# Kernel tuning notes

Measured on AMD Instinct MI355X. Metric: run time of the kernel, lower is better.

## Reference

```python
import jax, jax.numpy as jnp
import numpy as np

B, C, IN = 8, 1024, 256
OUT, H, NS, SD = 256, 4, 5, 64
DK = OUT // H


def setup_inputs() -> dict:
    key = jax.random.key(0)
    ks = jax.random.split(key, 16)
    s = lambda k, *shape: jax.random.normal(k, shape, dtype=jnp.float32) * 0.05
    return {
        "x": jax.random.normal(ks[0], (B, C, IN), dtype=jnp.float32),
        "A_prior": jax.random.uniform(ks[1], (C, C), dtype=jnp.float32),
        # lin_project
        "Wp": s(ks[2], IN, OUT), "bp": jnp.zeros((OUT,), jnp.float32),
        # stage_mlp: Linear(IN,128) -> ReLU -> Linear(128,NS)
        "Ws1": s(ks[3], IN, 128), "bs1": jnp.zeros((128,), jnp.float32),
        "Ws2": s(ks[4], 128, NS), "bs2": jnp.zeros((NS,), jnp.float32),
        # mlp_c: Linear(NS,SD) -> ReLU -> Linear(SD,SD)
        "Wc1": s(ks[5], NS, SD), "bc1": jnp.zeros((SD,), jnp.float32),
        "Wc2": s(ks[6], SD, SD), "bc2": jnp.zeros((SD,), jnp.float32),
        # att_scorer: Linear(2*DK+SD, 1, bias=False) -> weight vector
        "att_w": s(ks[7], 2 * DK + SD),
        "lam": jnp.ones((H,), jnp.float32),
    }


def reference(x, A_prior, Wp, bp, Ws1, bs1, Ws2, bs2, Wc1, bc1, Wc2, bc2, att_w, lam):
    # projection -> (B, C, H, DK)
    x_proj = (x @ Wp + bp).reshape(B, C, H, DK)
    # stage logits from mean-pooled features
    s_logits = jax.nn.relu(x.mean(axis=1) @ Ws1 + bs1) @ Ws2 + bs2  # (B, NS)
    s_prob = jax.nn.softmax(s_logits, axis=-1)
    c = jax.nn.relu(s_prob @ Wc1 + bc1) @ Wc2 + bc2  # (B, SD)
    # att_scorer is linear over cat([x_src, x_dst, c]); decompose weight to
    # avoid materializing the (B,C,C,H,2*DK+SD) concat tensor.
    w_src, w_dst, w_c = att_w[:DK], att_w[DK:2 * DK], att_w[2 * DK:]
    src_s = jnp.einsum('bjhd,d->bjh', x_proj, w_src)  # x_src[b,i,j] = x_proj[b,j]
    dst_s = jnp.einsum('bihd,d->bih', x_proj, w_dst)  # x_dst[b,i,j] = x_proj[b,i]
    c_s = c @ w_c                                      # (B,)
    e = jax.nn.leaky_relu(
        src_s[:, None, :, :] + dst_s[:, :, None, :] + c_s[:, None, None, None],
        negative_slope=0.2)                            # (B, C, C, H)
    prior = lam[None, None, None, :] * jnp.log(A_prior[None, :, :, None] + 1e-9)
    alpha = jax.nn.softmax(e + prior, axis=2)          # softmax over src j
    out = jnp.einsum('bijh,bjhd->bihd', alpha, x_proj).reshape(B, C, OUT)
    return out, s_logits
```

## Files before the change

kernel.cpp:

```cpp
#include <hip/hip_runtime.h>
#include <hip/hip_fp16.h>

typedef _Float16 f16x8 __attribute__((ext_vector_type(8)));
typedef _Float16 f16x4 __attribute__((ext_vector_type(4)));
typedef float f32x4 __attribute__((ext_vector_type(4)));

#define NB 8
#define NNS 5


__global__ __launch_bounds__(256) void k_prew(const float* __restrict__ Wp,
                                              __half* __restrict__ WpTh) {
  const int k = blockIdx.x;
  const int f = threadIdx.x;
  WpTh[(f << 8) + k] = __float2half(Wp[(k << 8) + f]);
}

__global__ __launch_bounds__(256) void k_mean(const float* __restrict__ x,
                                              float* __restrict__ xmean) {
  const int t = threadIdx.x;
  const int row0 = blockIdx.x << 5;
  const int b = row0 >> 10;
  float ps = 0.f;
  #pragma unroll 8
  for (int r = 0; r < 32; ++r) ps += x[(size_t)(row0 + r) * 256 + t];
  atomicAdd(&xmean[(b << 8) + t], ps);
}

__global__ __launch_bounds__(256, 4) void k_projM(
    const float* __restrict__ x, const __half* __restrict__ WpTh,
    const float* __restrict__ bp, const float* __restrict__ att_w,
    __half* __restrict__ xpT, float* __restrict__ srcP,
    float* __restrict__ dstT) {
  const int t = threadIdx.x;
  const int l = t & 63, w = t >> 6;
  const int lm = l & 15, q = l >> 4;
  const int bm = blockIdx.x >> 2, nh = blockIdx.x & 3;
  const int R0 = (bm << 6) + (w << 4);
  const int f0 = nh << 6;

  const float* arow = x + (size_t)(R0 + lm) * 256 + (q << 3);
  f16x8 ah[8];
  #pragma unroll
  for (int kk = 0; kk < 8; ++kk) {
    const f32x4 xa = *(const f32x4*)(arow + (kk << 5));
    const f32x4 xb = *(const f32x4*)(arow + (kk << 5) + 4);
    f16x8 v;
    #pragma unroll
    for (int u = 0; u < 4; ++u) {
      v[u] = (_Float16)xa[u];
      v[u + 4] = (_Float16)xb[u];
    }
    ah[kk] = v;
  }

  f32x4 acc[4];
  #pragma unroll
  for (int n = 0; n < 4; ++n) acc[n] = (f32x4){0.f, 0.f, 0.f, 0.f};
  #pragma unroll
  for (int n = 0; n < 4; ++n) {
    const __half* brow = WpTh + (size_t)(f0 + (n << 4) + lm) * 256 + (q << 3);
    #pragma unroll
    for (int kk = 0; kk < 8; ++kk) {
      const f16x8 bf = *(const f16x8*)(brow + (kk << 5));
      acc[n] = __builtin_amdgcn_mfma_f32_16x16x32_f16(ah[kk], bf, acc[n],
                                                      0, 0, 0);
    }
  }

  const int b = R0 >> 10;
  const int il = (R0 & 1023) + (q << 2);
  float wsn[4], wdn[4];
  #pragma unroll
  for (int n = 0; n < 4; ++n) {
    const int d = (n << 4) + lm;
    wsn[n] = att_w[d];
    wdn[n] = att_w[64 + d];
  }
  #pragma unroll
  for (int n = 0; n < 4; ++n) {
    const int f = f0 + (n << 4) + lm;
    const float bias = bp[f];
    f16x4 o;
    #pragma unroll
    for (int reg = 0; reg < 4; ++reg) {
      acc[n][reg] += bias;
      o[reg] = (_Float16)acc[n][reg];
    }
    *(f16x4*)(xpT + (((size_t)((b << 8) + f)) << 10) + il) = o;
  }
  #pragma unroll
  for (int reg = 0; reg < 4; ++reg) {
    float ss = 0.f, ds = 0.f;
    #pragma unroll
    for (int n = 0; n < 4; ++n) {
      ss = fmaf(acc[n][reg], wsn[n], ss);
      ds = fmaf(acc[n][reg], wdn[n], ds);
    }
    #pragma unroll
    for (int off = 1; off < 16; off <<= 1) {
      ss += __shfl_xor(ss, off);
      ds += __shfl_xor(ds, off);
    }
    if (lm == 0) {
      const int i = il + reg;
      srcP[((((b << 10) + i)) << 2) + nh] = ss;
      dstT[(((b << 2) + nh) << 10) + i] = ds;
    }
  }
}

__global__ __launch_bounds__(256) void k_head(
    const float* __restrict__ Ws1, const float* __restrict__ bs1,
    const float* __restrict__ Ws2, const float* __restrict__ bs2,
    const float* __restrict__ Wc1, const float* __restrict__ bc1,
    const float* __restrict__ Wc2, const float* __restrict__ bc2,
    const float* __restrict__ att_w, const float* __restrict__ xmean,
    float* __restrict__ cs_ws, float* __restrict__ out_slogits) {
  __shared__ float xm[256];
  __shared__ float h1[128];
  __shared__ float sl[NNS];
  __shared__ float sp[NNS];
  __shared__ float cc1[64];
  __shared__ float cvec[64];
  const int b = blockIdx.x, t = threadIdx.x;
  xm[t] = xmean[b * 256 + t] * (1.f / 1024.f);
  __syncthreads();
  if (t < 128) {
    float a = bs1[t];
    for (int f = 0; f < 256; ++f) a = fmaf(xm[f], Ws1[f * 128 + t], a);
    h1[t] = fmaxf(a, 0.f);
  }
  __syncthreads();
  if (t < NNS) {
    float a = bs2[t];
    for (int k = 0; k < 128; ++k) a = fmaf(h1[k], Ws2[k * NNS + t], a);
    sl[t] = a;
    out_slogits[b * NNS + t] = a;
  }
  __syncthreads();
  if (t == 0) {
    float m = sl[0];
    for (int n = 1; n < NNS; ++n) m = fmaxf(m, sl[n]);
    float s = 0.f;
    for (int n = 0; n < NNS; ++n) { sp[n] = expf(sl[n] - m); s += sp[n]; }
    for (int n = 0; n < NNS; ++n) sp[n] /= s;
  }
  __syncthreads();
  if (t < 64) {
    float a = bc1[t];
    for (int n = 0; n < NNS; ++n) a = fmaf(sp[n], Wc1[n * 64 + t], a);
    cc1[t] = fmaxf(a, 0.f);
  }
  __syncthreads();
  if (t < 64) {
    float a = bc2[t];
    for (int m = 0; m < 64; ++m) a = fmaf(cc1[m], Wc2[m * 64 + t], a);
    cvec[t] = a;
  }
  __syncthreads();
  if (t < 64) {
    float v = cvec[t] * att_w[128 + t];
    #pragma unroll
    for (int m = 32; m; m >>= 1) v += __shfl_xor(v, m);
    if (t == 0) cs_ws[b] = v;
  }
}

__global__ __launch_bounds__(512, 4) void k_attn(
    const __half* __restrict__ xpT, const float* __restrict__ A,
    const float* __restrict__ srcP, const float* __restrict__ dstT,
    const float* __restrict__ cs_ws, const float* __restrict__ lam,
    float* __restrict__ out) {
  __shared__ __align__(16) __half wl[4][16][256];
  __shared__ float dinv[4][16];
  const int t = threadIdx.x;
  const int l = t & 63;
  const int w = t >> 6;
  const int b = blockIdx.x >> 6;
  const int i0 = (blockIdx.x & 63) << 4;
  const float csv = cs_ws[b];
  float lam2[4], dstc[2][4];
  #pragma unroll
  for (int h = 0; h < 4; ++h) {
    lam2[h] = lam[h] * 0.69314718056f;
    #pragma unroll
    for (int rr = 0; rr < 2; ++rr)
      dstc[rr][h] = dstT[(((b << 2) + h) << 10) + i0 + 2 * w + rr] + csv;
  }
  const int r0g = i0 + 2 * w;
  const float* Ar0 = A + (size_t)r0g * 1024;
  const float* Ar1 = Ar0 + 1024;
  char* wlb = (char*)wl;

  const int h2 = w & 3, rh = w >> 2;
  const int lm = l & 15, q = l >> 4;
  f32x4 acc0 = {0.f, 0.f, 0.f, 0.f};
  f32x4 acc1 = {0.f, 0.f, 0.f, 0.f};
  const __half* xb0 =
      xpT + (((size_t)((b << 8) + (h2 << 6) + (rh << 5) + lm)) << 10);
  const __half* xb1 = xb0 + (16 << 10);

  float sums[2][4];
  #pragma unroll
  for (int rr = 0; rr < 2; ++rr)
    #pragma unroll
    for (int h = 0; h < 4; ++h) sums[rr][h] = 0.f;

  for (int cc = 0; cc < 4; ++cc) {
    #pragma unroll
    for (int st = 0; st < 2; ++st) {
      const int jl = (st << 7) + (l << 1);
      const int jg = (cc << 8) + jl;
      const float2 a0 = *(const float2*)(Ar0 + jg);
      const float2 a1 = *(const float2*)(Ar1 + jg);
      const f32x4 sv0 = *(const f32x4*)(srcP + (((b << 10) + jg) << 2));
      const f32x4 sv1 = *(const f32x4*)(srcP + (((b << 10) + jg + 1) << 2));
      float la[2][2];
      la[0][0] = __log2f(a0.x + 1e-9f);
      la[0][1] = __log2f(a0.y + 1e-9f);
      la[1][0] = __log2f(a1.x + 1e-9f);
      la[1][1] = __log2f(a1.y + 1e-9f);
      #pragma unroll
      for (int h = 0; h < 4; ++h) {
        #pragma unroll
        for (int rr = 0; rr < 2; ++rr) {
          __half2 pk;
          #pragma unroll
          for (int jj = 0; jj < 2; ++jj) {
            const float e = (jj ? sv1[h] : sv0[h]) + dstc[rr][h];
            const float lk = fmaxf(e, 0.2f * e);
            const float s = fmaf(lam2[h], la[rr][jj], lk);
            const float p = __expf(s);
            sums[rr][h] += p;
            if (jj) pk.y = __float2half(p); else pk.x = __float2half(p);
          }
          const int row = 2 * w + rr;
          *(__half2*)(wlb + (h << 13) + (row << 9) +
                      ((jl << 1) ^ ((row & 7) << 4))) = pk;
        }
      }
    }
    if (cc == 3) {
      #pragma unroll
      for (int rr = 0; rr < 2; ++rr)
        #pragma unroll
        for (int h = 0; h < 4; ++h) {
          float s = sums[rr][h];
          #pragma unroll
          for (int mm = 32; mm; mm >>= 1) s += __shfl_xor(s, mm);
          sums[rr][h] = s;
        }
      if (l == 0) {
        #pragma unroll
        for (int rr = 0; rr < 2; ++rr)
          #pragma unroll
          for (int h = 0; h < 4; ++h)
            dinv[h][2 * w + rr] = 1.f / sums[rr][h];
      }
    }
    __syncthreads();
    const char* ab = wlb + (h2 << 13) + (lm << 9);
    const int xa = (lm & 7) << 4;
    const __half* xb0c = xb0 + (cc << 8);
    const __half* xb1c = xb1 + (cc << 8);
    #pragma unroll
    for (int kk = 0; kk < 8; ++kk) {
      const int jl2 = (kk << 5) + (q << 3);
      const f16x8 af = *(const f16x8*)(ab + ((jl2 << 1) ^ xa));
      const f16x8 bf0 = *(const f16x8*)(xb0c + jl2);
      const f16x8 bf1 = *(const f16x8*)(xb1c + jl2);
      acc0 = __builtin_amdgcn_mfma_f32_16x16x32_f16(af, bf0, acc0, 0, 0, 0);
      acc1 = __builtin_amdgcn_mfma_f32_16x16x32_f16(af, bf1, acc1, 0, 0, 0);
    }
    __syncthreads();
  }
  float* ob =
      out + (((size_t)((b << 10) + i0)) << 8) + (h2 << 6) + (rh << 5) + lm;
  #pragma unroll
  for (int reg = 0; reg < 4; ++reg) {
    const int mrow = (q << 2) + reg;
    const float dv = dinv[h2][mrow];
    ob[(size_t)mrow << 8] = acc0[reg] * dv;
    ob[((size_t)mrow << 8) + 16] = acc1[reg] * dv;
  }
}

extern "C" void kernel_launch(void* const* d_in, const int* in_sizes, int n_in,
                              void* d_out, int out_size, void* d_ws,
                              size_t ws_size, hipStream_t stream) {
  const float* x     = (const float*)d_in[0];
  const float* A     = (const float*)d_in[1];
  const float* Wp    = (const float*)d_in[2];
  const float* bp    = (const float*)d_in[3];
  const float* Ws1   = (const float*)d_in[4];
  const float* bs1   = (const float*)d_in[5];
  const float* Ws2   = (const float*)d_in[6];
  const float* bs2   = (const float*)d_in[7];
  const float* Wc1   = (const float*)d_in[8];
  const float* bc1   = (const float*)d_in[9];
  const float* Wc2   = (const float*)d_in[10];
  const float* bc2   = (const float*)d_in[11];
  const float* att_w = (const float*)d_in[12];
  const float* lam   = (const float*)d_in[13];
  float* out = (float*)d_out;
  float* ws  = (float*)d_ws;

  __half* xpT  = (__half*)ws;
  float* srcP  = ws + 1048576;
  float* dstT  = ws + 1081344;
  float* xmean = ws + 1114112;
  float* cs    = ws + 1116160;
  __half* WpTh = (__half*)(ws + 1116168);

  hipMemsetAsync(xmean, 0, 2048 * sizeof(float), stream);

  k_prew<<<dim3(256), dim3(256), 0, stream>>>(Wp, WpTh);
  k_mean<<<dim3(256), dim3(256), 0, stream>>>(x, xmean);
  k_projM<<<dim3(512), dim3(256), 0, stream>>>(x, WpTh, bp, att_w, xpT, srcP,
                                               dstT);
  k_head<<<dim3(NB), dim3(256), 0, stream>>>(Ws1, bs1, Ws2, bs2, Wc1, bc1,
                                             Wc2, bc2, att_w, xmean, cs,
                                             out + NB * 1024 * 256);
  k_attn<<<dim3(512), dim3(512), 0, stream>>>(xpT, A, srcP, dstT, cs, lam,
                                              out);
}
```

Measured before the change: 159.5 us.

## Build attention weights in MFMA registers, dropping LDS staging and block syncs

The attention kernel now has each wave compute its softmax probabilities directly in the MFMA A-operand fragment for one head. Source scores move to a head-major layout so they can be loaded as contiguous vectors. This removes the shared-memory weight tile, the __syncthreads barriers and the LDS reduction of row sums; row normalisers are computed with shuffles instead. In exchange, the grid doubles and splits head dims across blocks, so the log/exp of the prior is recomputed per head and per half, which multiplies transcendental work and A-matrix reads. Separately, the weight-transpose and mean kernels are merged into one launch, and the head MLP's first layer is split across all 256 threads.

Measured after the change: 183.9 us. 15.3% more time.

```diff
diff --git a/kernel.cpp b/kernel.cpp
--- a/kernel.cpp
+++ b/kernel.cpp
@@ -9,28 +9,29 @@
 #define NNS 5
 
 
-__global__ __launch_bounds__(256) void k_prew(const float* __restrict__ Wp,
-                                              __half* __restrict__ WpTh) {
-  const int k = blockIdx.x;
-  const int f = threadIdx.x;
-  WpTh[(f << 8) + k] = __float2half(Wp[(k << 8) + f]);
-}
-
-__global__ __launch_bounds__(256) void k_mean(const float* __restrict__ x,
-                                              float* __restrict__ xmean) {
+__global__ __launch_bounds__(256) void k_pre(const float* __restrict__ Wp,
+                                             const float* __restrict__ x,
+                                             __half* __restrict__ WpTh,
+                                             float* __restrict__ xmean) {
   const int t = threadIdx.x;
-  const int row0 = blockIdx.x << 5;
-  const int b = row0 >> 10;
-  float ps = 0.f;
-  #pragma unroll 8
-  for (int r = 0; r < 32; ++r) ps += x[(size_t)(row0 + r) * 256 + t];
-  atomicAdd(&xmean[(b << 8) + t], ps);
+  int blk = blockIdx.x;
+  if (blk < 256) {
+    WpTh[(t << 8) + blk] = __float2half(Wp[(blk << 8) + t]);
+  } else {
+    blk -= 256;
+    const int row0 = blk << 5;
+    const int b = row0 >> 10;
+    float ps = 0.f;
+    #pragma unroll 8
+    for (int r = 0; r < 32; ++r) ps += x[(size_t)(row0 + r) * 256 + t];
+    atomicAdd(&xmean[(b << 8) + t], ps);
+  }
 }
 
 __global__ __launch_bounds__(256, 4) void k_projM(
     const float* __restrict__ x, const __half* __restrict__ WpTh,
     const float* __restrict__ bp, const float* __restrict__ att_w,
-    __half* __restrict__ xpT, float* __restrict__ srcP,
+    __half* __restrict__ xpT, float* __restrict__ srcT,
     float* __restrict__ dstT) {
   const int t = threadIdx.x;
   const int l = t & 63, w = t >> 6;
@@ -104,7 +105,7 @@
     }
     if (lm == 0) {
       const int i = il + reg;
-      srcP[((((b << 10) + i)) << 2) + nh] = ss;
+      srcT[(((b << 2) + nh) << 10) + i] = ss;
       dstT[(((b << 2) + nh) << 10) + i] = ds;
     }
   }
@@ -118,6 +119,7 @@
     const float* __restrict__ att_w, const float* __restrict__ xmean,
     float* __restrict__ cs_ws, float* __restrict__ out_slogits) {
   __shared__ float xm[256];
+  __shared__ float h1p[2][128];
   __shared__ float h1[128];
   __shared__ float sl[NNS];
   __shared__ float sp[NNS];
@@ -126,14 +128,21 @@
   const int b = blockIdx.x, t = threadIdx.x;
   xm[t] = xmean[b * 256 + t] * (1.f / 1024.f);
   __syncthreads();
-  if (t < 128) {
-    float a = bs1[t];
-    for (int f = 0; f < 256; ++f) a = fmaf(xm[f], Ws1[f * 128 + t], a);
-    h1[t] = fmaxf(a, 0.f);
-  }
+  {
+    const int kh = t >> 7, f = t & 127;
+    const float* wcol = Ws1 + (kh << 7) * 128 + f;
+    const float* xk = xm + (kh << 7);
+    float a = 0.f;
+    #pragma unroll 8
+    for (int k = 0; k < 128; ++k) a = fmaf(xk[k], wcol[k * 128], a);
+    h1p[kh][f] = a;
+  }
+  __syncthreads();
+  if (t < 128) h1[t] = fmaxf(h1p[0][t] + h1p[1][t] + bs1[t], 0.f);
   __syncthreads();
   if (t < NNS) {
     float a = bs2[t];
+    #pragma unroll 8
     for (int k = 0; k < 128; ++k) a = fmaf(h1[k], Ws2[k * NNS + t], a);
     sl[t] = a;
     out_slogits[b * NNS + t] = a;
@@ -149,12 +158,14 @@
   __syncthreads();
   if (t < 64) {
     float a = bc1[t];
+    #pragma unroll
     for (int n = 0; n < NNS; ++n) a = fmaf(sp[n], Wc1[n * 64 + t], a);
     cc1[t] = fmaxf(a, 0.f);
   }
   __syncthreads();
   if (t < 64) {
     float a = bc2[t];
+    #pragma unroll 8
     for (int m = 0; m < 64; ++m) a = fmaf(cc1[m], Wc2[m * 64 + t], a);
     cvec[t] = a;
   }
@@ -167,120 +178,76 @@
   }
 }
 
-__global__ __launch_bounds__(512, 4) void k_attn(
+__global__ __launch_bounds__(256, 4) void k_attn(
     const __half* __restrict__ xpT, const float* __restrict__ A,
-    const float* __restrict__ srcP, const float* __restrict__ dstT,
+    const float* __restrict__ srcT, const float* __restrict__ dstT,
     const float* __restrict__ cs_ws, const float* __restrict__ lam,
     float* __restrict__ out) {
-  __shared__ __align__(16) __half wl[4][16][256];
-  __shared__ float dinv[4][16];
   const int t = threadIdx.x;
-  const int l = t & 63;
-  const int w = t >> 6;
-  const int b = blockIdx.x >> 6;
-  const int i0 = (blockIdx.x & 63) << 4;
+  const int l = t & 63, h = t >> 6;
+  const int lm = l & 15, q = l >> 4;
+  const int blk = blockIdx.x;
+  const int b = blk >> 7;
+  const int tile = (blk >> 1) & 63;
+  const int dh = blk & 1;
+  const int i0 = tile << 4;
+
   const float csv = cs_ws[b];
-  float lam2[4], dstc[2][4];
-  #pragma unroll
-  for (int h = 0; h < 4; ++h) {
-    lam2[h] = lam[h] * 0.69314718056f;
-    #pragma unroll
-    for (int rr = 0; rr < 2; ++rr)
-      dstc[rr][h] = dstT[(((b << 2) + h) << 10) + i0 + 2 * w + rr] + csv;
-  }
-  const int r0g = i0 + 2 * w;
-  const float* Ar0 = A + (size_t)r0g * 1024;
-  const float* Ar1 = Ar0 + 1024;
-  char* wlb = (char*)wl;
-
-  const int h2 = w & 3, rh = w >> 2;
-  const int lm = l & 15, q = l >> 4;
+  const float lamln2 = lam[h] * 0.69314718056f;
+  const float dstc = dstT[(((b << 2) + h) << 10) + i0 + lm] + csv;
+  const float* Arow = A + (size_t)(i0 + lm) * 1024;
+  const float* srcb = srcT + (((b << 2) + h) << 10);
+  const __half* xb0 =
+      xpT + (((size_t)((b << 8) + (h << 6) + (dh << 5) + lm)) << 10);
+  const __half* xb1 = xb0 + (16 << 10);
+
   f32x4 acc0 = {0.f, 0.f, 0.f, 0.f};
   f32x4 acc1 = {0.f, 0.f, 0.f, 0.f};
-  const __half* xb0 =
-      xpT + (((size_t)((b << 8) + (h2 << 6) + (rh << 5) + lm)) << 10);
-  const __half* xb1 = xb0 + (16 << 10);
-
-  float sums[2][4];
-  #pragma unroll
-  for (int rr = 0; rr < 2; ++rr)
-    #pragma unroll
-    for (int h = 0; h < 4; ++h) sums[rr][h] = 0.f;
-
-  for (int cc = 0; cc < 4; ++cc) {
-    #pragma unroll
-    for (int st = 0; st < 2; ++st) {
-      const int jl = (st << 7) + (l << 1);
-      const int jg = (cc << 8) + jl;
-      const float2 a0 = *(const float2*)(Ar0 + jg);
-      const float2 a1 = *(const float2*)(Ar1 + jg);
-      const f32x4 sv0 = *(const f32x4*)(srcP + (((b << 10) + jg) << 2));
-      const f32x4 sv1 = *(const f32x4*)(srcP + (((b << 10) + jg + 1) << 2));
-      float la[2][2];
-      la[0][0] = __log2f(a0.x + 1e-9f);
-      la[0][1] = __log2f(a0.y + 1e-9f);
-      la[1][0] = __log2f(a1.x + 1e-9f);
-      la[1][1] = __log2f(a1.y + 1e-9f);
-      #pragma unroll
-      for (int h = 0; h < 4; ++h) {
-        #pragma unroll
-        for (int rr = 0; rr < 2; ++rr) {
-          __half2 pk;
-          #pragma unroll
-          for (int jj = 0; jj < 2; ++jj) {
-            const float e = (jj ? sv1[h] : sv0[h]) + dstc[rr][h];
-            const float lk = fmaxf(e, 0.2f * e);
-            const float s = fmaf(lam2[h], la[rr][jj], lk);
-            const float p = __expf(s);
-            sums[rr][h] += p;
-            if (jj) pk.y = __float2half(p); else pk.x = __float2half(p);
-          }
-          const int row = 2 * w + rr;
-          *(__half2*)(wlb + (h << 13) + (row << 9) +
-                      ((jl << 1) ^ ((row & 7) << 4))) = pk;
-        }
+  float sum = 0.f;
+
+  #pragma unroll 2
+  for (int kk = 0; kk < 32; ++kk) {
+    const int j0 = (kk << 5) + (q << 3);
+    const f32x4 a0 = *(const f32x4*)(Arow + j0);
+    const f32x4 a1 = *(const f32x4*)(Arow + j0 + 4);
+    const f32x4 s0 = *(const f32x4*)(srcb + j0);
+    const f32x4 s1 = *(const f32x4*)(srcb + j0 + 4);
+    const f16x8 bf0 = *(const f16x8*)(xb0 + j0);
+    const f16x8 bf1 = *(const f16x8*)(xb1 + j0);
+    f16x8 af;
+    #pragma unroll
+    for (int u = 0; u < 4; ++u) {
+      {
+        const float la = __log2f(a0[u] + 1e-9f);
+        const float e = s0[u] + dstc;
+        const float lk = fmaxf(e, 0.2f * e);
+        const float p = __expf(fmaf(lamln2, la, lk));
+        sum += p;
+        af[u] = (_Float16)p;
       }
-    }
-    if (cc == 3) {
-      #pragma unroll
-      for (int rr = 0; rr < 2; ++rr)
-        #pragma unroll
-        for (int h = 0; h < 4; ++h) {
-          float s = sums[rr][h];
-          #pragma unroll
-          for (int mm = 32; mm; mm >>= 1) s += __shfl_xor(s, mm);
-          sums[rr][h] = s;
-        }
-      if (l == 0) {
-        #pragma unroll
-        for (int rr = 0; rr < 2; ++rr)
-          #pragma unroll
-          for (int h = 0; h < 4; ++h)
-            dinv[h][2 * w + rr] = 1.f / sums[rr][h];
+      {
+        const float la = __log2f(a1[u] + 1e-9f);
+        const float e = s1[u] + dstc;
+        const float lk = fmaxf(e, 0.2f * e);
+        const float p = __expf(fmaf(lamln2, la, lk));
+        sum += p;
+        af[u + 4] = (_Float16)p;
       }
     }
-    __syncthreads();
-    const char* ab = wlb + (h2 << 13) + (lm << 9);
-    const int xa = (lm & 7) << 4;
-    const __half* xb0c = xb0 + (cc << 8);
-    const __half* xb1c = xb1 + (cc << 8);
-    #pragma unroll
-    for (int kk = 0; kk < 8; ++kk) {
-      const int jl2 = (kk << 5) + (q << 3);
-      const f16x8 af = *(const f16x8*)(ab + ((jl2 << 1) ^ xa));
-      const f16x8 bf0 = *(const f16x8*)(xb0c + jl2);
-      const f16x8 bf1 = *(const f16x8*)(xb1c + jl2);
-      acc0 = __builtin_amdgcn_mfma_f32_16x16x32_f16(af, bf0, acc0, 0, 0, 0);
-      acc1 = __builtin_amdgcn_mfma_f32_16x16x32_f16(af, bf1, acc1, 0, 0, 0);
-    }
-    __syncthreads();
-  }
+    acc0 = __builtin_amdgcn_mfma_f32_16x16x32_f16(af, bf0, acc0, 0, 0, 0);
+    acc1 = __builtin_amdgcn_mfma_f32_16x16x32_f16(af, bf1, acc1, 0, 0, 0);
+  }
+
+  sum += __shfl_xor(sum, 16);
+  sum += __shfl_xor(sum, 32);
+  const float dinv_l = 1.f / sum;
+
   float* ob =
-      out + (((size_t)((b << 10) + i0)) << 8) + (h2 << 6) + (rh << 5) + lm;
+      out + (((size_t)((b << 10) + i0)) << 8) + (h << 6) + (dh << 5) + lm;
   #pragma unroll
   for (int reg = 0; reg < 4; ++reg) {
     const int mrow = (q << 2) + reg;
-    const float dv = dinv[h2][mrow];
+    const float dv = __shfl(dinv_l, mrow);
     ob[(size_t)mrow << 8] = acc0[reg] * dv;
     ob[((size_t)mrow << 8) + 16] = acc1[reg] * dv;
   }
@@ -307,7 +274,7 @@
   float* ws  = (float*)d_ws;
 
   __half* xpT  = (__half*)ws;
-  float* srcP  = ws + 1048576;
+  float* srcT  = ws + 1048576;
   float* dstT  = ws + 1081344;
   float* xmean = ws + 1114112;
   float* cs    = ws + 1116160;
@@ -315,13 +282,12 @@
 
   hipMemsetAsync(xmean, 0, 2048 * sizeof(float), stream);
 
-  k_prew<<<dim3(256), dim3(256), 0, stream>>>(Wp, WpTh);
-  k_mean<<<dim3(256), dim3(256), 0, stream>>>(x, xmean);
-  k_projM<<<dim3(512), dim3(256), 0, stream>>>(x, WpTh, bp, att_w, xpT, srcP,
+  k_pre<<<dim3(512), dim3(256), 0, stream>>>(Wp, x, WpTh, xmean);
+  k_projM<<<dim3(512), dim3(256), 0, stream>>>(x, WpTh, bp, att_w, xpT, srcT,
                                                dstT);
   k_head<<<dim3(NB), dim3(256), 0, stream>>>(Ws1, bs1, Ws2, bs2, Wc1, bc1,
                                              Wc2, bc2, att_w, xmean, cs,
                                              out + NB * 1024 * 256);
-  k_attn<<<dim3(512), dim3(512), 0, stream>>>(xpT, A, srcP, dstT, cs, lam,
-                                              out);
-}
+  k_attn<<<dim3(1024), dim3(256), 0, stream>>>(xpT, A, srcT, dstT, cs, lam,
+                                               out);
+}
```
